# Kernel tuning notes

Measured on AMD Instinct MI355X. Metric: run time of the kernel, lower is better.

## Reference

```python
import jax, jax.numpy as jnp
import numpy as np

EPS = 1e-5

def gamma_layer_norm(x, gamma):
    # LayerNorm over last dim with learnable gamma only (no bias)
    mu = jnp.mean(x, axis=-1, keepdims=True)
    var = jnp.var(x, axis=-1, keepdims=True)
    return (x - mu) * jax.lax.rsqrt(var + EPS) * gamma

def setup_inputs() -> dict:
    key = jax.random.key(0)
    k1, k2, k3, k4 = jax.random.split(key, 4)
    b, n, dim = 8, 4096, 512
    heads, head_size = 8, 64
    hidden = heads * head_size  # 512
    x = jax.random.normal(k1, (b, n, dim), dtype=jnp.float32)
    # nn.Linear(dim, hidden*3, bias=False): weight [3*hidden, dim]
    w_qkv = jax.random.normal(k2, (3 * hidden, dim), dtype=jnp.float32) * (dim ** -0.5)
    # nn.Linear(hidden, dim, bias=False): weight [dim, hidden]
    w_out = jax.random.normal(k3, (dim, hidden), dtype=jnp.float32) * (hidden ** -0.5)
    gamma = 1.0 + 0.02 * jax.random.normal(k4, (dim,), dtype=jnp.float32)
    return {"x": x, "w_qkv": w_qkv, "w_out": w_out, "gamma": gamma}

def reference(x, w_qkv, w_out, gamma):
    b, n, dim = x.shape
    heads, head_size = 8, 64
    scale = head_size ** -0.5
    # norm=False -> Identity; no time conditioning
    qkv = jnp.einsum('bnd,hd->bnh', x, w_qkv)  # [b, n, 3*hidden]
    q, k, v = jnp.split(qkv, 3, axis=-1)
    def to_heads(t):
        return t.reshape(b, n, heads, head_size).transpose(0, 2, 1, 3)  # b h n d
    q, k, v = to_heads(q), to_heads(k), to_heads(v)
    q = jax.nn.softmax(q, axis=-1) * scale   # softmax over feature dim
    k = jax.nn.softmax(k, axis=-2)           # softmax over sequence dim
    context = jnp.einsum('bhnd,bhne->bhde', k, v)      # [b, h, d, e]
    out = jnp.einsum('bhde,bhnd->bhne', context, q)    # [b, h, n, e]
    out = out.transpose(0, 2, 1, 3).reshape(b, n, heads * head_size)
    out = jnp.einsum('bnh,dh->bnd', out, w_out)
    out = gamma_layer_norm(out, gamma)  # dropout inactive (p=0 / eval)
    return out
```

## Files before the change

kernel.cpp:

```cpp
#include <hip/hip_runtime.h>
#include <hip/hip_bf16.h>
#include <stdint.h>
#include <stddef.h>

typedef __bf16 bf16_t;
typedef __bf16 bf16x8 __attribute__((ext_vector_type(8)));
typedef float floatx4 __attribute__((ext_vector_type(4)));

#define DIM 512
#define SEQ 4096
#define BATCH 8

static __device__ __forceinline__ floatx4 mfma_bf16(bf16x8 a, bf16x8 b, floatx4 c) {
  return __builtin_amdgcn_mfma_f32_16x16x32_bf16(a, b, c, 0, 0, 0);
}

typedef __attribute__((address_space(1))) const void* gas_ptr;
typedef __attribute__((address_space(3))) void* las_ptr;
static __device__ __forceinline__ void gll16(const void* g, void* l) {
  __builtin_amdgcn_global_load_lds((gas_ptr)g, (las_ptr)l, 16, 0, 0);
}

__global__ __launch_bounds__(256) void k_cvt(const float* __restrict__ w, bf16_t* __restrict__ wb) {
  int i = (blockIdx.x * 256 + threadIdx.x) * 8;
  float4 a = *(const float4*)&w[i];
  float4 b = *(const float4*)&w[i + 4];
  bf16x8 o;
  o[0] = (bf16_t)a.x; o[1] = (bf16_t)a.y; o[2] = (bf16_t)a.z; o[3] = (bf16_t)a.w;
  o[4] = (bf16_t)b.x; o[5] = (bf16_t)b.y; o[6] = (bf16_t)b.z; o[7] = (bf16_t)b.w;
  *(bf16x8*)&wb[i] = o;
}

template<bool XB>
__global__ __launch_bounds__(256) void k_qkv(const float* __restrict__ X,
                                             const bf16_t* __restrict__ Xb,
                                             const bf16_t* __restrict__ Wb,
                                             bf16_t* __restrict__ qs,
                                             bf16_t* __restrict__ ek,
                                             bf16_t* __restrict__ vb,
                                             float* __restrict__ S) {
  __shared__ __align__(16) char Abuf[XB ? (128 * 64 * 2) : (128 * 64 * 4)];
  __shared__ __align__(16) bf16_t Bs[128 * 64];
  const int tid = threadIdx.x;
  const int lane = tid & 63;
  const int w = tid >> 6;
  const int wr = w >> 1, wc = w & 1;
  const int l15 = lane & 15, l4 = lane >> 4;
  const int m0 = blockIdx.x * 128;
  const int n0 = blockIdx.y * 128;

  const bf16_t* gB = Wb + (size_t)(n0 + w * 32 + (lane >> 3)) * DIM + (((lane & 7) ^ (lane >> 3)) << 3);
  bf16_t* lB = Bs + (w * 32) * 64 + lane * 8;

  const bf16_t* gAb = Xb + (size_t)(m0 + w * 32 + (lane >> 3)) * DIM + (((lane & 7) ^ (lane >> 3)) << 3);
  bf16_t* lAb = (bf16_t*)Abuf + (w * 32) * 64 + lane * 8;
  const int r4 = lane >> 4, uu = lane & 15;
  const float* gA0 = X + (size_t)(m0 + w * 32 + r4) * DIM + ((uu ^ r4) << 2);
  const float* gA1 = X + (size_t)(m0 + w * 32 + r4) * DIM + ((uu ^ (4 | r4)) << 2);
  float* lAf = (float*)Abuf + (w * 32) * 64 + lane * 4;

  floatx4 acc[4][4];
#pragma unroll
  for (int i = 0; i < 4; ++i)
#pragma unroll
    for (int j = 0; j < 4; ++j) acc[i][j] = (floatx4){0.f, 0.f, 0.f, 0.f};

  for (int kt = 0; kt < DIM; kt += 64) {
    if constexpr (XB) {
#pragma unroll
      for (int i = 0; i < 4; ++i) gll16(gAb + i * 8 * DIM, lAb + i * 8 * 64);
      gAb += 64;
    } else {
#pragma unroll
      for (int i = 0; i < 8; ++i) {
        const float* s = ((i & 1) ? gA1 : gA0) + i * 4 * DIM;
        gll16(s, lAf + i * 4 * 64);
      }
      gA0 += 64; gA1 += 64;
    }
#pragma unroll
    for (int i = 0; i < 4; ++i) gll16(gB + i * 8 * DIM, lB + i * 8 * 64);
    gB += 64;
    __syncthreads();
#pragma unroll
    for (int kk = 0; kk < 2; ++kk) {
      bf16x8 af[4], bfr[4];
#pragma unroll
      for (int f = 0; f < 4; ++f) {
        int ar = wr * 64 + f * 16 + l15;
        if constexpr (XB) {
          int ua = (kk * 4 + l4) ^ (l15 & 7);
          af[f] = *(const bf16x8*)((const bf16_t*)Abuf + ar * 64 + ua * 8);
        } else {
          int u0 = (kk * 8 + l4 * 2) ^ (l15 & 7);
          int u1 = (kk * 8 + l4 * 2 + 1) ^ (l15 & 7);
          float4 a0 = *(const float4*)((const float*)Abuf + ar * 64 + u0 * 4);
          float4 a1 = *(const float4*)((const float*)Abuf + ar * 64 + u1 * 4);
          bf16x8 t;
          t[0] = (bf16_t)a0.x; t[1] = (bf16_t)a0.y; t[2] = (bf16_t)a0.z; t[3] = (bf16_t)a0.w;
          t[4] = (bf16_t)a1.x; t[5] = (bf16_t)a1.y; t[6] = (bf16_t)a1.z; t[7] = (bf16_t)a1.w;
          af[f] = t;
        }
        int br = wc * 64 + f * 16 + l15;
        int ub = (kk * 4 + l4) ^ (l15 & 7);
        bfr[f] = *(const bf16x8*)(Bs + br * 64 + ub * 8);
      }
#pragma unroll
      for (int i = 0; i < 4; ++i)
#pragma unroll
        for (int j = 0; j < 4; ++j)
          acc[i][j] = mfma_bf16(af[i], bfr[j], acc[i][j]);
    }
    __syncthreads();
  }

  const int colbase = n0 + wc * 64;
  if (n0 < 512) {
#pragma unroll
    for (int fm = 0; fm < 4; ++fm) {
#pragma unroll
      for (int r = 0; r < 4; ++r) {
        float v0 = acc[fm][0][r], v1 = acc[fm][1][r], v2 = acc[fm][2][r], v3 = acc[fm][3][r];
        float mx = fmaxf(fmaxf(v0, v1), fmaxf(v2, v3));
        mx = fmaxf(mx, __shfl_xor(mx, 1));
        mx = fmaxf(mx, __shfl_xor(mx, 2));
        mx = fmaxf(mx, __shfl_xor(mx, 4));
        mx = fmaxf(mx, __shfl_xor(mx, 8));
        float e0 = __expf(v0 - mx), e1 = __expf(v1 - mx), e2 = __expf(v2 - mx), e3 = __expf(v3 - mx);
        float s = e0 + e1 + e2 + e3;
        s += __shfl_xor(s, 1); s += __shfl_xor(s, 2); s += __shfl_xor(s, 4); s += __shfl_xor(s, 8);
        float inv = 0.125f / s;
        int m = m0 + wr * 64 + fm * 16 + l4 * 4 + r;
        bf16_t* rowp = qs + (size_t)m * DIM + colbase;
        rowp[l15]      = (bf16_t)(e0 * inv);
        rowp[16 + l15] = (bf16_t)(e1 * inv);
        rowp[32 + l15] = (bf16_t)(e2 * inv);
        rowp[48 + l15] = (bf16_t)(e3 * inv);
      }
    }
  } else if (n0 < 1024) {
    const int cb = colbase - 512;
    float c0 = 0.f, c1 = 0.f, c2 = 0.f, c3 = 0.f;
#pragma unroll
    for (int fm = 0; fm < 4; ++fm) {
#pragma unroll
      for (int r = 0; r < 4; ++r) {
        int m = m0 + wr * 64 + fm * 16 + l4 * 4 + r;
        bf16_t* rowp = ek + (size_t)m * DIM + cb;
        float e0 = __expf(acc[fm][0][r]);
        float e1 = __expf(acc[fm][1][r]);
        float e2 = __expf(acc[fm][2][r]);
        float e3 = __expf(acc[fm][3][r]);
        rowp[l15]      = (bf16_t)e0;
        rowp[16 + l15] = (bf16_t)e1;
        rowp[32 + l15] = (bf16_t)e2;
        rowp[48 + l15] = (bf16_t)e3;
        c0 += e0; c1 += e1; c2 += e2; c3 += e3;
      }
    }
    c0 += __shfl_xor(c0, 16); c0 += __shfl_xor(c0, 32);
    c1 += __shfl_xor(c1, 16); c1 += __shfl_xor(c1, 32);
    c2 += __shfl_xor(c2, 16); c2 += __shfl_xor(c2, 32);
    c3 += __shfl_xor(c3, 16); c3 += __shfl_xor(c3, 32);
    if (lane < 16) {
      int b = m0 >> 12;
      atomicAdd(&S[b * 512 + cb + lane],      c0);
      atomicAdd(&S[b * 512 + cb + 16 + lane], c1);
      atomicAdd(&S[b * 512 + cb + 32 + lane], c2);
      atomicAdd(&S[b * 512 + cb + 48 + lane], c3);
    }
  } else {
    const int cb = colbase - 1024;
#pragma unroll
    for (int fm = 0; fm < 4; ++fm) {
#pragma unroll
      for (int r = 0; r < 4; ++r) {
        int m = m0 + wr * 64 + fm * 16 + l4 * 4 + r;
        bf16_t* rowp = vb + (size_t)m * DIM + cb;
        rowp[l15]      = (bf16_t)acc[fm][0][r];
        rowp[16 + l15] = (bf16_t)acc[fm][1][r];
        rowp[32 + l15] = (bf16_t)acc[fm][2][r];
        rowp[48 + l15] = (bf16_t)acc[fm][3][r];
      }
    }
  }
}

#define TP 136
__global__ __launch_bounds__(256) void k_ctx(const bf16_t* __restrict__ ek,
                                             const bf16_t* __restrict__ vb,
                                             float* __restrict__ ctxpart) {
  __shared__ __align__(16) bf16_t ekT[64 * TP];
  __shared__ __align__(16) bf16_t vT[64 * TP];
  __shared__ float red[4096];
  const int tid = threadIdx.x;
  const int lane = tid & 63, wid = tid >> 6;
  const int l15 = lane & 15, l4 = lane >> 4;
  const int bh = blockIdx.x, chunk = blockIdx.y;
  const int b = bh >> 3, h = bh & 7;
  const int base = b * SEQ + chunk * 512;

  floatx4 acc[4][4];
#pragma unroll
  for (int i = 0; i < 4; ++i)
#pragma unroll
    for (int j = 0; j < 4; ++j) acc[i][j] = (floatx4){0.f, 0.f, 0.f, 0.f};

  for (int nt = 0; nt < 4; ++nt) {
    const int n0 = base + nt * 128;
#pragma unroll
    for (int i = 0; i < 4; ++i) {
      int q = tid + i * 256;
      int n = q & 127;
      int c8 = (q >> 7) << 3;
      bf16x8 vk = *(const bf16x8*)&ek[(size_t)(n0 + n) * DIM + h * 64 + c8];
      bf16x8 vv = *(const bf16x8*)&vb[(size_t)(n0 + n) * DIM + h * 64 + c8];
#pragma unroll
      for (int j = 0; j < 8; ++j) {
        ekT[(c8 + j) * TP + n] = vk[j];
        vT [(c8 + j) * TP + n] = vv[j];
      }
    }
    __syncthreads();
    const int nb = wid * 32;
    bf16x8 af[4], bfr[4];
#pragma unroll
    for (int f = 0; f < 4; ++f) {
      af[f]  = *(const bf16x8*)&ekT[(f * 16 + l15) * TP + nb + l4 * 8];
      bfr[f] = *(const bf16x8*)&vT [(f * 16 + l15) * TP + nb + l4 * 8];
    }
#pragma unroll
    for (int i = 0; i < 4; ++i)
#pragma unroll
      for (int j = 0; j < 4; ++j)
        acc[i][j] = mfma_bf16(af[i], bfr[j], acc[i][j]);
    __syncthreads();
  }

  for (int w = 0; w < 4; ++w) {
    if (wid == w) {
#pragma unroll
      for (int fm = 0; fm < 4; ++fm)
#pragma unroll
        for (int fn = 0; fn < 4; ++fn)
#pragma unroll
          for (int r = 0; r < 4; ++r) {
            int d = fm * 16 + l4 * 4 + r;
            int e = fn * 16 + l15;
            if (w == 0) red[d * 64 + e] = acc[fm][fn][r];
            else        red[d * 64 + e] += acc[fm][fn][r];
          }
    }
    __syncthreads();
  }
  float* dst = ctxpart + ((size_t)bh * 8 + chunk) * 4096;
#pragma unroll
  for (int i = 0; i < 4; ++i) {
    int q = tid + i * 256;
    *(float4*)&dst[q * 4] = *(const float4*)&red[q * 4];
  }
}

__global__ __launch_bounds__(256) void k_ctxred(const float* __restrict__ ctxpart,
                                                const float* __restrict__ S,
                                                float* __restrict__ ctx) {
  int bh = blockIdx.x;
  int idx = blockIdx.y * 256 + threadIdx.x;
  int b = bh >> 3, h = bh & 7;
  float s = 0.f;
#pragma unroll
  for (int p = 0; p < 8; ++p) s += ctxpart[((size_t)bh * 8 + p) * 4096 + idx];
  int d = idx >> 6;
  ctx[(size_t)bh * 4096 + idx] = s / S[b * 512 + h * 64 + d];
}

__global__ __launch_bounds__(128) void k_mt(const float* __restrict__ ctx,
                                            const float* __restrict__ w_out,
                                            bf16_t* __restrict__ Mt) {
  __shared__ float cs[4096];
  const int tid = threadIdx.x;
  const int b = blockIdx.x, h = blockIdx.y, dq = blockIdx.z;
#pragma unroll
  for (int i = 0; i < 8; ++i) {
    int q = tid + i * 128;
    *(float4*)&cs[q * 4] = *(const float4*)&ctx[((size_t)(b * 8 + h)) * 4096 + q * 4];
  }
  __syncthreads();
  const int dcol = dq * 128 + tid;
  float a[64];
#pragma unroll
  for (int d = 0; d < 64; ++d) a[d] = 0.f;
  for (int e = 0; e < 64; ++e) {
    float we = w_out[(size_t)dcol * 512 + h * 64 + e];
#pragma unroll
    for (int d = 0; d < 64; ++d) a[d] += cs[d * 64 + e] * we;
  }
  bf16_t* dst = Mt + ((size_t)b * 512 + dcol) * 512 + h * 64;
#pragma unroll
  for (int g = 0; g < 8; ++g) {
    bf16x8 o;
#pragma unroll
    for (int j = 0; j < 8; ++j) o[j] = (bf16_t)a[g * 8 + j];
    *(bf16x8*)&dst[g * 8] = o;
  }
}

__global__ __launch_bounds__(256) void k_out(const bf16_t* __restrict__ qs,
                                             const bf16_t* __restrict__ Mt,
                                             bf16_t* __restrict__ out2b) {
  __shared__ __align__(16) bf16_t As[128 * 64];
  __shared__ __align__(16) bf16_t Bs[128 * 64];
  const int tid = threadIdx.x;
  const int lane = tid & 63, w = tid >> 6;
  const int wr = w >> 1, wc = w & 1;
  const int l15 = lane & 15, l4 = lane >> 4;
  const int m0 = blockIdx.x * 128;
  const int n0 = blockIdx.y * 128;
  const bf16_t* Bp = Mt + (size_t)(blockIdx.x >> 5) * 512 * 512;

  const bf16_t* gA = qs + (size_t)(m0 + w * 32 + (lane >> 3)) * 512 + (((lane & 7) ^ (lane >> 3)) << 3);
  const bf16_t* gB = Bp + (size_t)(n0 + w * 32 + (lane >> 3)) * 512 + (((lane & 7) ^ (lane >> 3)) << 3);
  bf16_t* lA = As + (w * 32) * 64 + lane * 8;
  bf16_t* lB = Bs + (w * 32) * 64 + lane * 8;

  floatx4 acc[4][4];
#pragma unroll
  for (int i = 0; i < 4; ++i)
#pragma unroll
    for (int j = 0; j < 4; ++j) acc[i][j] = (floatx4){0.f, 0.f, 0.f, 0.f};

  for (int kt = 0; kt < 512; kt += 64) {
#pragma unroll
    for (int i = 0; i < 4; ++i) {
      gll16(gA + i * 8 * 512, lA + i * 8 * 64);
      gll16(gB + i * 8 * 512, lB + i * 8 * 64);
    }
    gA += 64; gB += 64;
    __syncthreads();
#pragma unroll
    for (int kk = 0; kk < 2; ++kk) {
      bf16x8 af[4], bfr[4];
#pragma unroll
      for (int f = 0; f < 4; ++f) {
        int ar = wr * 64 + f * 16 + l15;
        int ua = (kk * 4 + l4) ^ (l15 & 7);
        af[f] = *(const bf16x8*)(As + ar * 64 + ua * 8);
        int br = wc * 64 + f * 16 + l15;
        int ub = (kk * 4 + l4) ^ (l15 & 7);
        bfr[f] = *(const bf16x8*)(Bs + br * 64 + ub * 8);
      }
#pragma unroll
      for (int i = 0; i < 4; ++i)
#pragma unroll
        for (int j = 0; j < 4; ++j)
          acc[i][j] = mfma_bf16(af[i], bfr[j], acc[i][j]);
    }
    __syncthreads();
  }
#pragma unroll
  for (int fm = 0; fm < 4; ++fm) {
#pragma unroll
    for (int r = 0; r < 4; ++r) {
      int m = m0 + wr * 64 + fm * 16 + l4 * 4 + r;
      bf16_t* rowp = out2b + (size_t)m * 512 + n0 + wc * 64;
      rowp[l15]      = (bf16_t)acc[fm][0][r];
      rowp[16 + l15] = (bf16_t)acc[fm][1][r];
      rowp[32 + l15] = (bf16_t)acc[fm][2][r];
      rowp[48 + l15] = (bf16_t)acc[fm][3][r];
    }
  }
}

__global__ __launch_bounds__(256) void k_ln(const bf16_t* __restrict__ out2b,
                                            const float* __restrict__ gamma,
                                            float* __restrict__ out) {
  const int lane = threadIdx.x & 63;
  const int row = blockIdx.x * 4 + (threadIdx.x >> 6);
  bf16x8 v = *(const bf16x8*)(out2b + (size_t)row * 512 + lane * 8);
  float f[8];
#pragma unroll
  for (int j = 0; j < 8; ++j) f[j] = (float)v[j];
  float s = 0.f, q = 0.f;
#pragma unroll
  for (int j = 0; j < 8; ++j) { s += f[j]; q += f[j] * f[j]; }
#pragma unroll
  for (int m = 1; m <= 32; m <<= 1) { s += __shfl_xor(s, m); q += __shfl_xor(q, m); }
  float mean = s * (1.f / 512.f);
  float var = q * (1.f / 512.f) - mean * mean;
  float rstd = rsqrtf(var + 1e-5f);
  float4 g0 = ((const float4*)gamma)[lane * 2];
  float4 g1 = ((const float4*)gamma)[lane * 2 + 1];
  float4 o0, o1;
  o0.x = (f[0] - mean) * rstd * g0.x;
  o0.y = (f[1] - mean) * rstd * g0.y;
  o0.z = (f[2] - mean) * rstd * g0.z;
  o0.w = (f[3] - mean) * rstd * g0.w;
  o1.x = (f[4] - mean) * rstd * g1.x;
  o1.y = (f[5] - mean) * rstd * g1.y;
  o1.z = (f[6] - mean) * rstd * g1.z;
  o1.w = (f[7] - mean) * rstd * g1.w;
  float* y = out + (size_t)row * 512;
  ((float4*)y)[lane * 2]     = o0;
  ((float4*)y)[lane * 2 + 1] = o1;
}

extern "C" void kernel_launch(void* const* d_in, const int* in_sizes, int n_in,
                              void* d_out, int out_size, void* d_ws, size_t ws_size,
                              hipStream_t stream) {
  const float* x     = (const float*)d_in[0];
  const float* w_qkv = (const float*)d_in[1];
  const float* w_out = (const float*)d_in[2];
  const float* gamma = (const float*)d_in[3];
  float* out = (float*)d_out;
  char* ws = (char*)d_ws;

  bf16_t* qs      = (bf16_t*)(ws);
  bf16_t* ek      = (bf16_t*)(ws + 33554432);
  bf16_t* vb      = (bf16_t*)(ws + 67108864);
  bf16_t* wqkvb   = (bf16_t*)(ws + 100663296);
  float*  S       = (float*)(ws + 102236160);
  bf16_t* Xb      = (bf16_t*)(ws + 102252544);
  float*  ctx     = (float*)(ws + 102252544);
  float*  ctxpart = (float*)(ws + 103301120);
  bf16_t* Mt      = (bf16_t*)(ws + 111689728);
  bf16_t* out2b   = (bf16_t*)(ws + 33554432);

  const bool big = ws_size >= (size_t)135806976;

  hipMemsetAsync(S, 0, BATCH * 512 * sizeof(float), stream);

  k_cvt<<<384, 256, 0, stream>>>(w_qkv, wqkvb);

  dim3 g1(256, 12);
  if (big) {
    k_cvt<<<8192, 256, 0, stream>>>(x, Xb);
    k_qkv<true><<<g1, 256, 0, stream>>>(x, Xb, wqkvb, qs, ek, vb, S);
  } else {
    k_qkv<false><<<g1, 256, 0, stream>>>(x, (const bf16_t*)nullptr, wqkvb, qs, ek, vb, S);
  }

  dim3 g2(64, 8);
  k_ctx<<<g2, 256, 0, stream>>>(ek, vb, ctxpart);

  dim3 g3(64, 16);
  k_ctxred<<<g3, 256, 0, stream>>>(ctxpart, S, ctx);

  dim3 g4(8, 8, 4);
  k_mt<<<g4, 128, 0, stream>>>(ctx, w_out, Mt);

  dim3 g5(256, 4);
  k_out<<<g5, 256, 0, stream>>>(qs, Mt, out2b);

  k_ln<<<8192, 256, 0, stream>>>(out2b, gamma, out);
}
```

Measured before the change: 198.8 us.

## Enlarge GEMM tiles to 256x256 with 512 threads and fuse ctx reduction into k_mt

The QKV and output-projection GEMMs move from 128x128 tiles on 4 waves to 256x256 tiles on 8 waves, each wave computing a 128x64 sub-tile. This doubles operand reuse per LDS load and cuts global traffic and block count. The separate context-reduction kernel is folded into k_mt, which now sums the partials and normalizes before the projection, saving one launch and one round trip through memory. The fp32-X fallback path is removed, so the workspace must always be large enough for Xb. The bigger tiles raise register pressure, with 128 accumulator floats per thread, and leave only 768 and 256 blocks on the GPU.

```diff
diff --git a/kernel.cpp b/kernel.cpp
--- a/kernel.cpp
+++ b/kernel.cpp
@@ -31,82 +31,60 @@
   *(bf16x8*)&wb[i] = o;
 }
 
-template<bool XB>
-__global__ __launch_bounds__(256) void k_qkv(const float* __restrict__ X,
-                                             const bf16_t* __restrict__ Xb,
-                                             const bf16_t* __restrict__ Wb,
-                                             bf16_t* __restrict__ qs,
-                                             bf16_t* __restrict__ ek,
-                                             bf16_t* __restrict__ vb,
-                                             float* __restrict__ S) {
-  __shared__ __align__(16) char Abuf[XB ? (128 * 64 * 2) : (128 * 64 * 4)];
-  __shared__ __align__(16) bf16_t Bs[128 * 64];
+__global__ __launch_bounds__(512, 2) void k_qkv(const bf16_t* __restrict__ Xb,
+                                                const bf16_t* __restrict__ Wb,
+                                                bf16_t* __restrict__ qs,
+                                                bf16_t* __restrict__ ek,
+                                                bf16_t* __restrict__ vb,
+                                                float* __restrict__ S) {
+  __shared__ __align__(16) bf16_t As[256 * 64];
+  __shared__ __align__(16) bf16_t Bs[256 * 64];
   const int tid = threadIdx.x;
   const int lane = tid & 63;
   const int w = tid >> 6;
-  const int wr = w >> 1, wc = w & 1;
+  const int wr = w >> 2, wc = w & 3;
   const int l15 = lane & 15, l4 = lane >> 4;
-  const int m0 = blockIdx.x * 128;
-  const int n0 = blockIdx.y * 128;
-
-  const bf16_t* gB = Wb + (size_t)(n0 + w * 32 + (lane >> 3)) * DIM + (((lane & 7) ^ (lane >> 3)) << 3);
-  bf16_t* lB = Bs + (w * 32) * 64 + lane * 8;
-
-  const bf16_t* gAb = Xb + (size_t)(m0 + w * 32 + (lane >> 3)) * DIM + (((lane & 7) ^ (lane >> 3)) << 3);
-  bf16_t* lAb = (bf16_t*)Abuf + (w * 32) * 64 + lane * 8;
-  const int r4 = lane >> 4, uu = lane & 15;
-  const float* gA0 = X + (size_t)(m0 + w * 32 + r4) * DIM + ((uu ^ r4) << 2);
-  const float* gA1 = X + (size_t)(m0 + w * 32 + r4) * DIM + ((uu ^ (4 | r4)) << 2);
-  float* lAf = (float*)Abuf + (w * 32) * 64 + lane * 4;
-
-  floatx4 acc[4][4];
-#pragma unroll
-  for (int i = 0; i < 4; ++i)
+  const int m0 = blockIdx.x * 256;
+  const int n0 = blockIdx.y * 256;
+
+  const int srow = tid >> 3;
+  const int sunit = (tid & 7) ^ (srow & 7);
+  const bf16_t* gA = Xb + (size_t)(m0 + srow) * DIM + (sunit << 3);
+  const bf16_t* gB = Wb + (size_t)(n0 + srow) * DIM + (sunit << 3);
+  bf16_t* lA = As + tid * 8;
+  bf16_t* lB = Bs + tid * 8;
+
+  floatx4 acc[8][4];
+#pragma unroll
+  for (int i = 0; i < 8; ++i)
 #pragma unroll
     for (int j = 0; j < 4; ++j) acc[i][j] = (floatx4){0.f, 0.f, 0.f, 0.f};
 
   for (int kt = 0; kt < DIM; kt += 64) {
-    if constexpr (XB) {
-#pragma unroll
-      for (int i = 0; i < 4; ++i) gll16(gAb + i * 8 * DIM, lAb + i * 8 * 64);
-      gAb += 64;
-    } else {
-#pragma unroll
-      for (int i = 0; i < 8; ++i) {
-        const float* s = ((i & 1) ? gA1 : gA0) + i * 4 * DIM;
-        gll16(s, lAf + i * 4 * 64);
-      }
-      gA0 += 64; gA1 += 64;
-    }
-#pragma unroll
-    for (int i = 0; i < 4; ++i) gll16(gB + i * 8 * DIM, lB + i * 8 * 64);
-    gB += 64;
+#pragma unroll
+    for (int i = 0; i < 4; ++i) {
+      gll16(gA + (size_t)i * 64 * DIM, lA + i * 64 * 64);
+      gll16(gB + (size_t)i * 64 * DIM, lB + i * 64 * 64);
+    }
+    gA += 64; gB += 64;
     __syncthreads();
 #pragma unroll
     for (int kk = 0; kk < 2; ++kk) {
-      bf16x8 af[4], bfr[4];
+      bf16x8 af[8], bfr[4];
+#pragma unroll
+      for (int f = 0; f < 8; ++f) {
+        int ar = wr * 128 + f * 16 + l15;
+        int ua = (kk * 4 + l4) ^ (ar & 7);
+        af[f] = *(const bf16x8*)(As + ar * 64 + ua * 8);
+      }
 #pragma unroll
       for (int f = 0; f < 4; ++f) {
-        int ar = wr * 64 + f * 16 + l15;
-        if constexpr (XB) {
-          int ua = (kk * 4 + l4) ^ (l15 & 7);
-          af[f] = *(const bf16x8*)((const bf16_t*)Abuf + ar * 64 + ua * 8);
-        } else {
-          int u0 = (kk * 8 + l4 * 2) ^ (l15 & 7);
-          int u1 = (kk * 8 + l4 * 2 + 1) ^ (l15 & 7);
-          float4 a0 = *(const float4*)((const float*)Abuf + ar * 64 + u0 * 4);
-          float4 a1 = *(const float4*)((const float*)Abuf + ar * 64 + u1 * 4);
-          bf16x8 t;
-          t[0] = (bf16_t)a0.x; t[1] = (bf16_t)a0.y; t[2] = (bf16_t)a0.z; t[3] = (bf16_t)a0.w;
-          t[4] = (bf16_t)a1.x; t[5] = (bf16_t)a1.y; t[6] = (bf16_t)a1.z; t[7] = (bf16_t)a1.w;
-          af[f] = t;
-        }
         int br = wc * 64 + f * 16 + l15;
-        int ub = (kk * 4 + l4) ^ (l15 & 7);
+        int ub = (kk * 4 + l4) ^ (br & 7);
         bfr[f] = *(const bf16x8*)(Bs + br * 64 + ub * 8);
       }
 #pragma unroll
-      for (int i = 0; i < 4; ++i)
+      for (int i = 0; i < 8; ++i)
 #pragma unroll
         for (int j = 0; j < 4; ++j)
           acc[i][j] = mfma_bf16(af[i], bfr[j], acc[i][j]);
@@ -117,7 +95,7 @@
   const int colbase = n0 + wc * 64;
   if (n0 < 512) {
 #pragma unroll
-    for (int fm = 0; fm < 4; ++fm) {
+    for (int fm = 0; fm < 8; ++fm) {
 #pragma unroll
       for (int r = 0; r < 4; ++r) {
         float v0 = acc[fm][0][r], v1 = acc[fm][1][r], v2 = acc[fm][2][r], v3 = acc[fm][3][r];
@@ -130,7 +108,7 @@
         float s = e0 + e1 + e2 + e3;
         s += __shfl_xor(s, 1); s += __shfl_xor(s, 2); s += __shfl_xor(s, 4); s += __shfl_xor(s, 8);
         float inv = 0.125f / s;
-        int m = m0 + wr * 64 + fm * 16 + l4 * 4 + r;
+        int m = m0 + wr * 128 + fm * 16 + l4 * 4 + r;
         bf16_t* rowp = qs + (size_t)m * DIM + colbase;
         rowp[l15]      = (bf16_t)(e0 * inv);
         rowp[16 + l15] = (bf16_t)(e1 * inv);
@@ -142,10 +120,10 @@
     const int cb = colbase - 512;
     float c0 = 0.f, c1 = 0.f, c2 = 0.f, c3 = 0.f;
 #pragma unroll
-    for (int fm = 0; fm < 4; ++fm) {
+    for (int fm = 0; fm < 8; ++fm) {
 #pragma unroll
       for (int r = 0; r < 4; ++r) {
-        int m = m0 + wr * 64 + fm * 16 + l4 * 4 + r;
+        int m = m0 + wr * 128 + fm * 16 + l4 * 4 + r;
         bf16_t* rowp = ek + (size_t)m * DIM + cb;
         float e0 = __expf(acc[fm][0][r]);
         float e1 = __expf(acc[fm][1][r]);
@@ -172,10 +150,10 @@
   } else {
     const int cb = colbase - 1024;
 #pragma unroll
-    for (int fm = 0; fm < 4; ++fm) {
+    for (int fm = 0; fm < 8; ++fm) {
 #pragma unroll
       for (int r = 0; r < 4; ++r) {
-        int m = m0 + wr * 64 + fm * 16 + l4 * 4 + r;
+        int m = m0 + wr * 128 + fm * 16 + l4 * 4 + r;
         bf16_t* rowp = vb + (size_t)m * DIM + cb;
         rowp[l15]      = (bf16_t)acc[fm][0][r];
         rowp[16 + l15] = (bf16_t)acc[fm][1][r];
@@ -261,96 +239,96 @@
   }
 }
 
-__global__ __launch_bounds__(256) void k_ctxred(const float* __restrict__ ctxpart,
-                                                const float* __restrict__ S,
-                                                float* __restrict__ ctx) {
-  int bh = blockIdx.x;
-  int idx = blockIdx.y * 256 + threadIdx.x;
-  int b = bh >> 3, h = bh & 7;
-  float s = 0.f;
-#pragma unroll
-  for (int p = 0; p < 8; ++p) s += ctxpart[((size_t)bh * 8 + p) * 4096 + idx];
-  int d = idx >> 6;
-  ctx[(size_t)bh * 4096 + idx] = s / S[b * 512 + h * 64 + d];
-}
-
-__global__ __launch_bounds__(128) void k_mt(const float* __restrict__ ctx,
+__global__ __launch_bounds__(256) void k_mt(const float* __restrict__ ctxpart,
+                                            const float* __restrict__ S,
                                             const float* __restrict__ w_out,
                                             bf16_t* __restrict__ Mt) {
   __shared__ float cs[4096];
   const int tid = threadIdx.x;
-  const int b = blockIdx.x, h = blockIdx.y, dq = blockIdx.z;
-#pragma unroll
-  for (int i = 0; i < 8; ++i) {
-    int q = tid + i * 128;
-    *(float4*)&cs[q * 4] = *(const float4*)&ctx[((size_t)(b * 8 + h)) * 4096 + q * 4];
+  const int bh = blockIdx.x;
+  const int b = bh >> 3, h = bh & 7;
+#pragma unroll
+  for (int i = 0; i < 16; ++i) {
+    int idx = tid + i * 256;
+    float s = 0.f;
+#pragma unroll
+    for (int p = 0; p < 8; ++p) s += ctxpart[((size_t)bh * 8 + p) * 4096 + idx];
+    cs[idx] = s / S[b * 512 + h * 64 + (idx >> 6)];
   }
   __syncthreads();
-  const int dcol = dq * 128 + tid;
-  float a[64];
-#pragma unroll
-  for (int d = 0; d < 64; ++d) a[d] = 0.f;
-  for (int e = 0; e < 64; ++e) {
-    float we = w_out[(size_t)dcol * 512 + h * 64 + e];
-#pragma unroll
-    for (int d = 0; d < 64; ++d) a[d] += cs[d * 64 + e] * we;
-  }
-  bf16_t* dst = Mt + ((size_t)b * 512 + dcol) * 512 + h * 64;
-#pragma unroll
-  for (int g = 0; g < 8; ++g) {
-    bf16x8 o;
-#pragma unroll
-    for (int j = 0; j < 8; ++j) o[j] = (bf16_t)a[g * 8 + j];
-    *(bf16x8*)&dst[g * 8] = o;
-  }
-}
-
-__global__ __launch_bounds__(256) void k_out(const bf16_t* __restrict__ qs,
-                                             const bf16_t* __restrict__ Mt,
-                                             bf16_t* __restrict__ out2b) {
-  __shared__ __align__(16) bf16_t As[128 * 64];
-  __shared__ __align__(16) bf16_t Bs[128 * 64];
+  for (int half = 0; half < 2; ++half) {
+    const int dcol = half * 256 + tid;
+    float a[64];
+#pragma unroll
+    for (int d = 0; d < 64; ++d) a[d] = 0.f;
+    for (int e = 0; e < 64; ++e) {
+      float we = w_out[(size_t)dcol * 512 + h * 64 + e];
+#pragma unroll
+      for (int d = 0; d < 64; ++d) a[d] += cs[d * 64 + e] * we;
+    }
+    bf16_t* dst = Mt + ((size_t)b * 512 + dcol) * 512 + h * 64;
+#pragma unroll
+    for (int g = 0; g < 8; ++g) {
+      bf16x8 o;
+#pragma unroll
+      for (int j = 0; j < 8; ++j) o[j] = (bf16_t)a[g * 8 + j];
+      *(bf16x8*)&dst[g * 8] = o;
+    }
+  }
+}
+
+__global__ __launch_bounds__(512, 2) void k_out(const bf16_t* __restrict__ qs,
+                                                const bf16_t* __restrict__ Mt,
+                                                bf16_t* __restrict__ out2b) {
+  __shared__ __align__(16) bf16_t As[256 * 64];
+  __shared__ __align__(16) bf16_t Bs[256 * 64];
   const int tid = threadIdx.x;
-  const int lane = tid & 63, w = tid >> 6;
-  const int wr = w >> 1, wc = w & 1;
+  const int lane = tid & 63;
+  const int w = tid >> 6;
+  const int wr = w >> 2, wc = w & 3;
   const int l15 = lane & 15, l4 = lane >> 4;
-  const int m0 = blockIdx.x * 128;
-  const int n0 = blockIdx.y * 128;
-  const bf16_t* Bp = Mt + (size_t)(blockIdx.x >> 5) * 512 * 512;
-
-  const bf16_t* gA = qs + (size_t)(m0 + w * 32 + (lane >> 3)) * 512 + (((lane & 7) ^ (lane >> 3)) << 3);
-  const bf16_t* gB = Bp + (size_t)(n0 + w * 32 + (lane >> 3)) * 512 + (((lane & 7) ^ (lane >> 3)) << 3);
-  bf16_t* lA = As + (w * 32) * 64 + lane * 8;
-  bf16_t* lB = Bs + (w * 32) * 64 + lane * 8;
-
-  floatx4 acc[4][4];
-#pragma unroll
-  for (int i = 0; i < 4; ++i)
+  const int m0 = blockIdx.x * 256;
+  const int n0 = blockIdx.y * 256;
+  const bf16_t* Bp = Mt + (size_t)(blockIdx.x >> 4) * 512 * 512;
+
+  const int srow = tid >> 3;
+  const int sunit = (tid & 7) ^ (srow & 7);
+  const bf16_t* gA = qs + (size_t)(m0 + srow) * 512 + (sunit << 3);
+  const bf16_t* gB = Bp + (size_t)(n0 + srow) * 512 + (sunit << 3);
+  bf16_t* lA = As + tid * 8;
+  bf16_t* lB = Bs + tid * 8;
+
+  floatx4 acc[8][4];
+#pragma unroll
+  for (int i = 0; i < 8; ++i)
 #pragma unroll
     for (int j = 0; j < 4; ++j) acc[i][j] = (floatx4){0.f, 0.f, 0.f, 0.f};
 
   for (int kt = 0; kt < 512; kt += 64) {
 #pragma unroll
     for (int i = 0; i < 4; ++i) {
-      gll16(gA + i * 8 * 512, lA + i * 8 * 64);
-      gll16(gB + i * 8 * 512, lB + i * 8 * 64);
+      gll16(gA + (size_t)i * 64 * 512, lA + i * 64 * 64);
+      gll16(gB + (size_t)i * 64 * 512, lB + i * 64 * 64);
     }
     gA += 64; gB += 64;
     __syncthreads();
 #pragma unroll
     for (int kk = 0; kk < 2; ++kk) {
-      bf16x8 af[4], bfr[4];
+      bf16x8 af[8], bfr[4];
+#pragma unroll
+      for (int f = 0; f < 8; ++f) {
+        int ar = wr * 128 + f * 16 + l15;
+        int ua = (kk * 4 + l4) ^ (ar & 7);
+        af[f] = *(const bf16x8*)(As + ar * 64 + ua * 8);
+      }
 #pragma unroll
       for (int f = 0; f < 4; ++f) {
-        int ar = wr * 64 + f * 16 + l15;
-        int ua = (kk * 4 + l4) ^ (l15 & 7);
-        af[f] = *(const bf16x8*)(As + ar * 64 + ua * 8);
         int br = wc * 64 + f * 16 + l15;
-        int ub = (kk * 4 + l4) ^ (l15 & 7);
+        int ub = (kk * 4 + l4) ^ (br & 7);
         bfr[f] = *(const bf16x8*)(Bs + br * 64 + ub * 8);
       }
 #pragma unroll
-      for (int i = 0; i < 4; ++i)
+      for (int i = 0; i < 8; ++i)
 #pragma unroll
         for (int j = 0; j < 4; ++j)
           acc[i][j] = mfma_bf16(af[i], bfr[j], acc[i][j]);
@@ -358,10 +336,10 @@
     __syncthreads();
   }
 #pragma unroll
-  for (int fm = 0; fm < 4; ++fm) {
+  for (int fm = 0; fm < 8; ++fm) {
 #pragma unroll
     for (int r = 0; r < 4; ++r) {
-      int m = m0 + wr * 64 + fm * 16 + l4 * 4 + r;
+      int m = m0 + wr * 128 + fm * 16 + l4 * 4 + r;
       bf16_t* rowp = out2b + (size_t)m * 512 + n0 + wc * 64;
       rowp[l15]      = (bf16_t)acc[fm][0][r];
       rowp[16 + l15] = (bf16_t)acc[fm][1][r];
@@ -420,36 +398,25 @@
   bf16_t* wqkvb   = (bf16_t*)(ws + 100663296);
   float*  S       = (float*)(ws + 102236160);
   bf16_t* Xb      = (bf16_t*)(ws + 102252544);
-  float*  ctx     = (float*)(ws + 102252544);
   float*  ctxpart = (float*)(ws + 103301120);
   bf16_t* Mt      = (bf16_t*)(ws + 111689728);
   bf16_t* out2b   = (bf16_t*)(ws + 33554432);
 
-  const bool big = ws_size >= (size_t)135806976;
-
   hipMemsetAsync(S, 0, BATCH * 512 * sizeof(float), stream);
 
   k_cvt<<<384, 256, 0, stream>>>(w_qkv, wqkvb);
-
-  dim3 g1(256, 12);
-  if (big) {
-    k_cvt<<<8192, 256, 0, stream>>>(x, Xb);
-    k_qkv<true><<<g1, 256, 0, stream>>>(x, Xb, wqkvb, qs, ek, vb, S);
-  } else {
-    k_qkv<false><<<g1, 256, 0, stream>>>(x, (const bf16_t*)nullptr, wqkvb, qs, ek, vb, S);
-  }
+  k_cvt<<<8192, 256, 0, stream>>>(x, Xb);
+
+  dim3 g1(128, 6);
+  k_qkv<<<g1, 512, 0, stream>>>(Xb, wqkvb, qs, ek, vb, S);
 
   dim3 g2(64, 8);
   k_ctx<<<g2, 256, 0, stream>>>(ek, vb, ctxpart);
 
-  dim3 g3(64, 16);
-  k_ctxred<<<g3, 256, 0, stream>>>(ctxpart, S, ctx);
-
-  dim3 g4(8, 8, 4);
-  k_mt<<<g4, 128, 0, stream>>>(ctx, w_out, Mt);
-
-  dim3 g5(256, 4);
-  k_out<<<g5, 256, 0, stream>>>(qs, Mt, out2b);
+  k_mt<<<64, 256, 0, stream>>>(ctxpart, S, w_out, Mt);
+
+  dim3 g5(128, 2);
+  k_out<<<g5, 512, 0, stream>>>(qs, Mt, out2b);
 
   k_ln<<<8192, 256, 0, stream>>>(out2b, gamma, out);
 }
```

After: 219.9 us. 10.6% more time.
